# Optimization experiments

Measured on AMD Instinct MI355X. Metric: run time of the kernel, lower is better.

The kernel has to match this reference:

```python
import jax, jax.numpy as jnp
import numpy as np

D = 1024
H = 16
HD = D // H
FF = 4 * D
EPS = 1e-5


def _layernorm(x, g, s):
    m = x.mean(-1, keepdims=True)
    v = ((x - m) ** 2).mean(-1, keepdims=True)  # unbiased=False
    return g * (x - m) / jnp.sqrt(v + EPS) + s


def _gelu_tanh(x):
    c = jnp.sqrt(2.0 / jnp.pi).astype(x.dtype)
    return 0.5 * x * (1 + jnp.tanh(c * (x + 0.044715 * x ** 3)))


def setup_inputs() -> dict:
    key = jax.random.key(0)
    ks = jax.random.split(key, 12)
    B, T = 2, 2048
    std = 0.02
    x = jax.random.normal(ks[0], (B, T, D), jnp.float32)
    wq = jax.random.normal(ks[1], (D, D), jnp.float32) * std
    wk = jax.random.normal(ks[2], (D, D), jnp.float32) * std
    wv = jax.random.normal(ks[3], (D, D), jnp.float32) * std
    wo = jax.random.normal(ks[4], (D, D), jnp.float32) * std
    bo = jnp.zeros((D,), jnp.float32)
    w1 = jax.random.normal(ks[5], (FF, D), jnp.float32) * std
    b1 = jnp.zeros((FF,), jnp.float32)
    w2 = jax.random.normal(ks[6], (D, FF), jnp.float32) * std
    b2 = jnp.zeros((D,), jnp.float32)
    g1 = jnp.ones((D,), jnp.float32)
    s1 = jnp.zeros((D,), jnp.float32)
    g2 = jnp.ones((D,), jnp.float32)
    s2 = jnp.zeros((D,), jnp.float32)
    return {"x": x, "wq": wq, "wk": wk, "wv": wv, "wo": wo, "bo": bo,
            "w1": w1, "b1": b1, "w2": w2, "b2": b2,
            "g1": g1, "s1": s1, "g2": g2, "s2": s2}


def reference(x, wq, wk, wv, wo, bo, w1, b1, w2, b2, g1, s1, g2, s2):
    B, T, _ = x.shape
    # pre-LN attention
    h = _layernorm(x, g1, s1)
    q = (h @ wq.T).reshape(B, T, H, HD).transpose(0, 2, 1, 3)  # [B,H,T,HD]
    k = (h @ wk.T).reshape(B, T, H, HD).transpose(0, 2, 1, 3)
    v = (h @ wv.T).reshape(B, T, H, HD).transpose(0, 2, 1, 3)
    scores = jnp.einsum('bhqd,bhkd->bhqk', q, k)
    causal = jnp.triu(jnp.ones((T, T), bool), k=1)
    scores = jnp.where(causal, -jnp.inf, scores)
    attn = jax.nn.softmax(scores / jnp.sqrt(jnp.float32(HD)), axis=-1)
    ctx = jnp.einsum('bhqk,bhkd->bhqd', attn, v)
    ctx = ctx.transpose(0, 2, 1, 3).reshape(B, T, D)
    x = x + (ctx @ wo.T + bo)
    # pre-LN MLP
    h2 = _layernorm(x, g2, s2)
    ff = _gelu_tanh(h2 @ w1.T + b1) @ w2.T + b2
    return x + ff
```

## Files before the change

### kernel.cpp

```cpp
#include <hip/hip_runtime.h>
#include <hip/hip_bf16.h>
#include <stdint.h>


typedef __attribute__((ext_vector_type(8))) __bf16 bf16x8;
typedef __attribute__((ext_vector_type(4))) __bf16 bf16x4;
typedef __attribute__((ext_vector_type(4))) float  f32x4;

#define DD    1024
#define TSEQ  2048
#define NTOK  4096
#define FFD   4096

#define ASM_VMCNT0() asm volatile("s_waitcnt vmcnt(0)" ::: "memory")

__device__ __forceinline__ void gll16(const void* g, void* l) {
  __builtin_amdgcn_global_load_lds(
      (const __attribute__((address_space(1))) unsigned int*)g,
      (__attribute__((address_space(3))) unsigned int*)l, 16, 0, 0);
}

__device__ __forceinline__ float gelu_f(float v) {
  float u = 0.7978845608028654f * (v + 0.044715f * v * v * v);
  float t = 1.0f - 2.0f / (1.0f + __expf(2.0f * u));
  return 0.5f * v * (1.0f + t);
}

__global__ __launch_bounds__(256) void cvt_weights(
    const float* __restrict__ wq, const float* __restrict__ wk,
    const float* __restrict__ wv, const float* __restrict__ wo,
    const float* __restrict__ w1, const float* __restrict__ w2,
    __bf16* __restrict__ dst)
{
  size_t i4 = (size_t)blockIdx.x * 256 + threadIdx.x;
  size_t e = i4 * 4;
  const float* src; size_t off;
  if (e < (size_t)4 * 1048576) {
    int sel = (int)(e >> 20);
    src = sel == 0 ? wq : sel == 1 ? wk : sel == 2 ? wv : wo;
    off = e & 1048575;
  } else if (e < (size_t)8 * 1048576) {
    src = w1; off = e - (size_t)4 * 1048576;
  } else {
    src = w2; off = e - (size_t)8 * 1048576;
  }
  float4 v = *(const float4*)(src + off);
  bf16x4 o;
  o[0] = (__bf16)v.x; o[1] = (__bf16)v.y; o[2] = (__bf16)v.z; o[3] = (__bf16)v.w;
  *(bf16x4*)(dst + e) = o;
}

__global__ __launch_bounds__(256) void ln_kernel(
    const float* __restrict__ x, const float* __restrict__ gw,
    const float* __restrict__ sw, __bf16* __restrict__ out)
{
  const int row  = blockIdx.x * 4 + (threadIdx.x >> 6);
  const int lane = threadIdx.x & 63;
  const float4* xr = (const float4*)(x + (size_t)row * DD);
  float4 v[4];
  float s = 0.f, sq = 0.f;
#pragma unroll
  for (int i = 0; i < 4; ++i) {
    v[i] = xr[i * 64 + lane];
    s  += v[i].x + v[i].y + v[i].z + v[i].w;
    sq += v[i].x * v[i].x + v[i].y * v[i].y + v[i].z * v[i].z + v[i].w * v[i].w;
  }
#pragma unroll
  for (int off = 32; off >= 1; off >>= 1) {
    s  += __shfl_xor(s, off);
    sq += __shfl_xor(sq, off);
  }
  const float mean = s * (1.f / DD);
  const float rstd = rsqrtf(sq * (1.f / DD) - mean * mean + 1e-5f);
  const float4* gr = (const float4*)gw;
  const float4* sr = (const float4*)sw;
#pragma unroll
  for (int i = 0; i < 4; ++i) {
    float4 gv = gr[i * 64 + lane];
    float4 sv = sr[i * 64 + lane];
    bf16x4 o;
    o[0] = (__bf16)(gv.x * (v[i].x - mean) * rstd + sv.x);
    o[1] = (__bf16)(gv.y * (v[i].y - mean) * rstd + sv.y);
    o[2] = (__bf16)(gv.z * (v[i].z - mean) * rstd + sv.z);
    o[3] = (__bf16)(gv.w * (v[i].w - mean) * rstd + sv.w);
    *(bf16x4*)&out[(size_t)row * DD + (size_t)(i * 64 + lane) * 4] = o;
  }
}

template<int MODE>
__global__ __launch_bounds__(512, 2)
void gemm256(const __bf16* __restrict__ A, int lda,
             const __bf16* __restrict__ Bw, int ldb,
             __bf16* __restrict__ Cout, const float* __restrict__ bias,
             __bf16* __restrict__ voutT, int M, int N, int K)
{
  __shared__ __bf16 sm[65536];
  const int t = threadIdx.x;
  const int lane = t & 63;
  const int l15 = lane & 15, g = lane >> 4;
  const int w = t >> 6;
  const int wm = w >> 2, wn = w & 3;
  const int m0 = blockIdx.y * 256, n0 = blockIdx.x * 256;

  if (MODE == 2) {
    const int kz = blockIdx.z;
    A    += (size_t)kz * 1024;
    Bw   += (size_t)kz * 1024;
    Cout += (size_t)kz * (size_t)M * N;
  }

  const int srow = t >> 3;
  const int schunk = t & 7;
  const int gc = schunk ^ (srow & 7);
  const __bf16* gA = A  + (size_t)(m0 + srow) * lda + gc * 8;
  const __bf16* gB = Bw + (size_t)(n0 + srow) * ldb + gc * 8;
  char* smb = (char*)sm;
  const int sdst = t * 16;

  auto STAGE = [&](int kt, int cur) {
    char* dA = smb + cur * 65536;
    char* dB = dA + 32768;
    const __bf16* a = gA + kt * 64;
    const __bf16* b = gB + kt * 64;
#pragma unroll
    for (int i = 0; i < 4; ++i)
      gll16(a + (size_t)i * 64 * lda, dA + i * 8192 + sdst);
#pragma unroll
    for (int i = 0; i < 4; ++i)
      gll16(b + (size_t)i * 64 * ldb, dB + i * 8192 + sdst);
  };

  const int xa = l15 & 7;
  const int baseA0 = (wm * 128 + l15) * 128 + ((g ^ xa) << 4);
  const int baseA1 = (wm * 128 + l15) * 128 + (((4 + g) ^ xa) << 4);
  const int baseB0 = 32768 + (wn * 64 + l15) * 128 + ((g ^ xa) << 4);
  const int baseB1 = 32768 + (wn * 64 + l15) * 128 + (((4 + g) ^ xa) << 4);

  f32x4 acc[8][4] = {};
  const int NT = K >> 6;

  STAGE(0, 0);
  __syncthreads();

  for (int kt = 0; kt < NT; ++kt) {
    const int cur = kt & 1;
    if (kt + 1 < NT) STAGE(kt + 1, cur ^ 1);

    const char* bufb = smb + cur * 65536;
    bf16x8 af[8][2], bfr[4][2];
#pragma unroll
    for (int mi = 0; mi < 8; ++mi) {
      af[mi][0] = *(const bf16x8*)(bufb + baseA0 + mi * 2048);
      af[mi][1] = *(const bf16x8*)(bufb + baseA1 + mi * 2048);
    }
#pragma unroll
    for (int ni = 0; ni < 4; ++ni) {
      bfr[ni][0] = *(const bf16x8*)(bufb + baseB0 + ni * 2048);
      bfr[ni][1] = *(const bf16x8*)(bufb + baseB1 + ni * 2048);
    }
#pragma unroll
    for (int ks = 0; ks < 2; ++ks)
#pragma unroll
      for (int mi = 0; mi < 8; ++mi)
#pragma unroll
        for (int ni = 0; ni < 4; ++ni)
          acc[mi][ni] = __builtin_amdgcn_mfma_f32_16x16x32_bf16(
              af[mi][ks], bfr[ni][ks], acc[mi][ni], 0, 0, 0);

    __syncthreads();
  }

#pragma unroll
  for (int mi = 0; mi < 8; ++mi) {
    const int rr0 = m0 + wm * 128 + mi * 16 + 4 * g;
#pragma unroll
    for (int ni = 0; ni < 4; ++ni) {
      const int cc = n0 + wn * 64 + ni * 16 + l15;
      if (MODE == 0 && n0 + wn * 64 >= 2048) {
        const int b  = rr0 >> 11;
        const int t0 = rr0 & 2047;
        const int vc = cc - 2048;
        const int h = vc >> 6, d = vc & 63;
        bf16x4 o;
        o[0] = (__bf16)acc[mi][ni][0]; o[1] = (__bf16)acc[mi][ni][1];
        o[2] = (__bf16)acc[mi][ni][2]; o[3] = (__bf16)acc[mi][ni][3];
        *(bf16x4*)&voutT[(((size_t)(b * 16 + h)) * 64 + d) * 2048 + t0] = o;
      } else {
        const int ldc = (MODE == 0) ? 2048 : N;
#pragma unroll
        for (int r = 0; r < 4; ++r) {
          float v = acc[mi][ni][r];
          if (MODE == 0 && cc < 1024) v *= 0.125f;
          if (MODE == 1) { v += bias[cc]; v = gelu_f(v); }
          Cout[(size_t)(rr0 + r) * ldc + cc] = (__bf16)v;
        }
      }
    }
  }
}

__global__ __launch_bounds__(256) void ff2_reduce(
    const __bf16* __restrict__ part, const float* __restrict__ x2,
    const float* __restrict__ b2, float* __restrict__ out)
{
  const size_t e = ((size_t)blockIdx.x * 256 + threadIdx.x) * 4;
  float4 r = *(const float4*)(x2 + e);
  const float4 b = *(const float4*)(b2 + (e & 1023));
  r.x += b.x; r.y += b.y; r.z += b.z; r.w += b.w;
#pragma unroll
  for (int s = 0; s < 4; ++s) {
    bf16x4 p = *(const bf16x4*)(part + (size_t)s * 4194304 + e);
    r.x += (float)p[0]; r.y += (float)p[1]; r.z += (float)p[2]; r.w += (float)p[3];
  }
  *(float4*)(out + e) = r;
}

template<bool BIAS, bool RES>
__global__ __launch_bounds__(256, 3)
void gemm_bt(const __bf16* __restrict__ A, const __bf16* __restrict__ Bw,
             float* __restrict__ Cout, const float* __restrict__ bias,
             const float* __restrict__ res, int M, int N, int K)
{
  __shared__ __bf16 As[128 * 64];
  __shared__ __bf16 Bs[128 * 64];
  const int t    = threadIdx.x;
  const int lane = t & 63;
  const int l15  = lane & 15;
  const int g    = lane >> 4;
  const int w    = t >> 6;
  const int wr   = w >> 1, wc = w & 1;
  const int m0 = blockIdx.y * 128;
  const int n0 = blockIdx.x * 128;
  const int srow = t >> 3;
  const int scol = (t & 7) * 8;

  f32x4 acc[4][4] = {};
  const __bf16* Ap = A  + (size_t)m0 * K;
  const __bf16* Bp = Bw + (size_t)n0 * K;

  for (int k0 = 0; k0 < K; k0 += 64) {
#pragma unroll
    for (int i = 0; i < 4; ++i) {
      const int row = i * 32 + srow;
      gll16(Ap + (size_t)row * K + k0 + scol, &As[row * 64 + scol]);
    }
#pragma unroll
    for (int i = 0; i < 4; ++i) {
      const int row = i * 32 + srow;
      gll16(Bp + (size_t)row * K + k0 + scol, &Bs[row * 64 + scol]);
    }
    __syncthreads();
#pragma unroll
    for (int ks = 0; ks < 2; ++ks) {
      bf16x8 af[4], bfr[4];
#pragma unroll
      for (int mi = 0; mi < 4; ++mi)
        af[mi] = *(const bf16x8*)&As[(wr * 64 + mi * 16 + l15) * 64 + ks * 32 + g * 8];
#pragma unroll
      for (int ni = 0; ni < 4; ++ni)
        bfr[ni] = *(const bf16x8*)&Bs[(wc * 64 + ni * 16 + l15) * 64 + ks * 32 + g * 8];
#pragma unroll
      for (int mi = 0; mi < 4; ++mi)
#pragma unroll
        for (int ni = 0; ni < 4; ++ni)
          acc[mi][ni] = __builtin_amdgcn_mfma_f32_16x16x32_bf16(af[mi], bfr[ni], acc[mi][ni], 0, 0, 0);
    }
    __syncthreads();
  }

  const int crow0 = m0 + wr * 64;
  const int ccol0 = n0 + wc * 64;
#pragma unroll
  for (int mi = 0; mi < 4; ++mi) {
#pragma unroll
    for (int r = 0; r < 4; ++r) {
      const int rr = crow0 + mi * 16 + 4 * g + r;
#pragma unroll
      for (int ni = 0; ni < 4; ++ni) {
        const int cc = ccol0 + ni * 16 + l15;
        float v = acc[mi][ni][r];
        if (BIAS) v += bias[cc];
        if (RES)  v += res[(size_t)rr * N + cc];
        Cout[(size_t)rr * N + cc] = v;
      }
    }
  }
}

__device__ __forceinline__ void attn_tile(
    int kt, int qt, int qg,
    bf16x8 qf0, bf16x8 qf1,
    f32x4 (&acc)[4], float& mrun, float& lrun,
    char* pw, const char* KsB, const char* VTsB,
    int g, int l15, int xr)
{
  f32x4 s[4];
#pragma unroll
  for (int f = 0; f < 4; ++f) {
    const char* kb = KsB + (f * 16 + l15) * 128;
    bf16x8 a0 = *(const bf16x8*)(kb + ((g << 4) ^ xr));
    bf16x8 a1 = *(const bf16x8*)(kb + (((4 + g) << 4) ^ xr));
    f32x4 z = {};
    z = __builtin_amdgcn_mfma_f32_16x16x32_bf16(a0, qf0, z, 0, 0, 0);
    z = __builtin_amdgcn_mfma_f32_16x16x32_bf16(a1, qf1, z, 0, 0, 0);
    s[f] = z;
  }

  float pmax = -1e30f;
  if (kt == qt) {
#pragma unroll
    for (int f = 0; f < 4; ++f)
#pragma unroll
      for (int r = 0; r < 4; ++r) {
        const int kg = kt * 64 + f * 16 + g * 4 + r;
        if (kg > qg) s[f][r] = -1e30f;
        pmax = fmaxf(pmax, s[f][r]);
      }
  } else {
#pragma unroll
    for (int f = 0; f < 4; ++f)
#pragma unroll
      for (int r = 0; r < 4; ++r) pmax = fmaxf(pmax, s[f][r]);
  }
  pmax = fmaxf(pmax, __shfl_xor(pmax, 16));
  pmax = fmaxf(pmax, __shfl_xor(pmax, 32));

  if (__any(pmax > mrun)) {
    const float mnew  = fmaxf(mrun, pmax);
    const float alpha = __expf(mrun - mnew);
    float al[4];
#pragma unroll
    for (int r = 0; r < 4; ++r) al[r] = __shfl(alpha, g * 4 + r);
#pragma unroll
    for (int nf = 0; nf < 4; ++nf)
#pragma unroll
      for (int r = 0; r < 4; ++r) acc[nf][r] *= al[r];
    lrun *= alpha;
    mrun = mnew;
  }

  float lsum = 0.f;
#pragma unroll
  for (int f = 0; f < 4; ++f)
#pragma unroll
    for (int r = 0; r < 4; ++r) {
      float p = __expf(s[f][r] - mrun);
      s[f][r] = p;
      lsum += p;
    }
  lsum += __shfl_xor(lsum, 16);
  lsum += __shfl_xor(lsum, 32);
  lrun += lsum;

#pragma unroll
  for (int f = 0; f < 4; ++f) {
    bf16x4 pk;
    pk[0] = (__bf16)s[f][0]; pk[1] = (__bf16)s[f][1];
    pk[2] = (__bf16)s[f][2]; pk[3] = (__bf16)s[f][3];
    *(bf16x4*)(pw + ((((f * 2 + (g >> 1)) << 4) ^ xr) + (g & 1) * 8)) = pk;
  }
  asm volatile("s_waitcnt lgkmcnt(0)" ::: "memory");

#pragma unroll
  for (int ks = 0; ks < 2; ++ks) {
    bf16x8 pa = *(const bf16x8*)(pw + (((ks * 4 + g) << 4) ^ xr));
#pragma unroll
    for (int nf = 0; nf < 4; ++nf) {
      const char* vb = VTsB + (nf * 16 + l15) * 128;
      bf16x8 vf = *(const bf16x8*)(vb + (((ks * 4 + g) << 4) ^ xr));
      acc[nf] = __builtin_amdgcn_mfma_f32_16x16x32_bf16(pa, vf, acc[nf], 0, 0, 0);
    }
  }
}

__global__ __launch_bounds__(256, 2)
void attn_kernel(const __bf16* __restrict__ qk, const __bf16* __restrict__ vT,
                 __bf16* __restrict__ ctx)
{
  __shared__ __bf16 Ks[64 * 64];
  __shared__ __bf16 VTs[64 * 64];
  __shared__ __bf16 Ps[4][2][1024];
  const int t    = threadIdx.x;
  const int lane = t & 63;
  const int l15  = lane & 15;
  const int g    = lane >> 4;
  const int w    = t >> 6;
  const int j  = blockIdx.x;
  const int qtA = j, qtB = 31 - j;
  const int hh = blockIdx.y;
  const int bb = blockIdx.z;

  const int qrowA = qtA * 64 + w * 16 + l15;
  const int qrowB = qtB * 64 + w * 16 + l15;
  const size_t qkrA = ((size_t)(bb * 2048 + qrowA)) * 2048 + hh * 64;
  const size_t qkrB = ((size_t)(bb * 2048 + qrowB)) * 2048 + hh * 64;
  bf16x8 qfA0 = *(const bf16x8*)&qk[qkrA + g * 8];
  bf16x8 qfA1 = *(const bf16x8*)&qk[qkrA + 32 + g * 8];
  bf16x8 qfB0 = *(const bf16x8*)&qk[qkrB + g * 8];
  bf16x8 qfB1 = *(const bf16x8*)&qk[qkrB + 32 + g * 8];

  const int kk = t >> 2;
  const int c0 = (t & 3) * 16;
  const __bf16* kbase = &qk[((size_t)(bb * 2048) + kk) * 2048 + 1024 + hh * 64 + c0];
  const __bf16* vbase = &vT[(((size_t)(bb * 16 + hh)) * 64 + kk) * 2048 + c0];
  const int xw  = (kk & 7) << 4;
  char* kdst = (char*)Ks  + kk * 128;
  char* vdst = (char*)VTs + kk * 128;
  const int cw0 = ((((t & 3) * 2)    ) << 4) ^ xw;
  const int cw1 = ((((t & 3) * 2) + 1) << 4) ^ xw;

  f32x4 accA[4] = {}, accB[4] = {};
  float mA = -1e30f, lA = 0.f, mB = -1e30f, lB = 0.f;
  const int qgA = qtA * 64 + w * 16 + l15;
  const int qgB = qtB * 64 + w * 16 + l15;

  bf16x8 ka0, ka1, va0, va1, kb0, kb1, vb0, vb1;

  auto LOAD = [&](int kt, bf16x8& k0, bf16x8& k1, bf16x8& v0, bf16x8& v1) {
    const __bf16* kp = kbase + (size_t)kt * 64 * 2048;
    k0 = *(const bf16x8*)(kp);
    k1 = *(const bf16x8*)(kp + 8);
    const __bf16* vp = vbase + kt * 64;
    v0 = *(const bf16x8*)(vp);
    v1 = *(const bf16x8*)(vp + 8);
  };
  auto WRITE = [&](bf16x8& k0, bf16x8& k1, bf16x8& v0, bf16x8& v1) {
    *(bf16x8*)(kdst + cw0) = k0;
    *(bf16x8*)(kdst + cw1) = k1;
    *(bf16x8*)(vdst + cw0) = v0;
    *(bf16x8*)(vdst + cw1) = v1;
  };

  const int xr = (l15 & 7) << 4;
  char* pwA = (char*)&Ps[w][0][0] + l15 * 128;
  char* pwB = (char*)&Ps[w][1][0] + l15 * 128;
  const char* KsB  = (const char*)Ks;
  const char* VTsB = (const char*)VTs;

  const int NT = qtB + 1;
  LOAD(0, ka0, ka1, va0, va1);
  int kt = 0;
  for (;;) {
    ASM_VMCNT0();
    __syncthreads();
    WRITE(ka0, ka1, va0, va1);
    if (kt + 1 < NT) LOAD(kt + 1, kb0, kb1, vb0, vb1);
    __syncthreads();
    attn_tile(kt, qtB, qgB, qfB0, qfB1, accB, mB, lB, pwB, KsB, VTsB, g, l15, xr);
    if (kt <= qtA)
      attn_tile(kt, qtA, qgA, qfA0, qfA1, accA, mA, lA, pwA, KsB, VTsB, g, l15, xr);
    if (++kt >= NT) break;

    ASM_VMCNT0();
    __syncthreads();
    WRITE(kb0, kb1, vb0, vb1);
    if (kt + 1 < NT) LOAD(kt + 1, ka0, ka1, va0, va1);
    __syncthreads();
    attn_tile(kt, qtB, qgB, qfB0, qfB1, accB, mB, lB, pwB, KsB, VTsB, g, l15, xr);
    if (kt <= qtA)
      attn_tile(kt, qtA, qgA, qfA0, qfA1, accA, mA, lA, pwA, KsB, VTsB, g, l15, xr);
    if (++kt >= NT) break;
  }

  float liA[4], liB[4];
#pragma unroll
  for (int r = 0; r < 4; ++r) {
    liA[r] = 1.0f / __shfl(lA, g * 4 + r);
    liB[r] = 1.0f / __shfl(lB, g * 4 + r);
  }
#pragma unroll
  for (int nf = 0; nf < 4; ++nf)
#pragma unroll
    for (int r = 0; r < 4; ++r) {
      const int rowA = qtA * 64 + w * 16 + 4 * g + r;
      const int rowB = qtB * 64 + w * 16 + 4 * g + r;
      ctx[((size_t)(bb * 2048 + rowA)) * DD + hh * 64 + nf * 16 + l15] =
          (__bf16)(accA[nf][r] * liA[r]);
      ctx[((size_t)(bb * 2048 + rowB)) * DD + hh * 64 + nf * 16 + l15] =
          (__bf16)(accB[nf][r] * liB[r]);
    }
}

extern "C" void kernel_launch(void* const* d_in, const int* in_sizes, int n_in,
                              void* d_out, int out_size, void* d_ws, size_t ws_size,
                              hipStream_t stream)
{
  (void)in_sizes; (void)n_in; (void)out_size; (void)ws_size;
  const float* x  = (const float*)d_in[0];
  const float* wq = (const float*)d_in[1];
  const float* wk = (const float*)d_in[2];
  const float* wv = (const float*)d_in[3];
  const float* wo = (const float*)d_in[4];
  const float* bo = (const float*)d_in[5];
  const float* w1 = (const float*)d_in[6];
  const float* b1 = (const float*)d_in[7];
  const float* w2 = (const float*)d_in[8];
  const float* b2 = (const float*)d_in[9];
  const float* g1 = (const float*)d_in[10];
  const float* s1 = (const float*)d_in[11];
  const float* g2 = (const float*)d_in[12];
  const float* s2 = (const float*)d_in[13];
  float* out = (float*)d_out;

  char* ws = (char*)d_ws;
  __bf16* wbf  = (__bf16*)ws;
  __bf16* hbuf = (__bf16*)(ws + 25165824);
  __bf16* qkb  = (__bf16*)(ws + 33554432);
  __bf16* vbT  = (__bf16*)(ws + 50331648);
  __bf16* ctxb = (__bf16*)(ws + 58720256);
  float*  x2   = (float*)(ws + 67108864);
  __bf16* ffb  = (__bf16*)(ws + 83886080);
  __bf16* part = (__bf16*)(ws + 33554432);

  cvt_weights<<<12288, 256, 0, stream>>>(wq, wk, wv, wo, w1, w2, wbf);
  ln_kernel<<<1024, 256, 0, stream>>>(x, g1, s1, hbuf);

  gemm256<0><<<dim3(12, 16), 512, 0, stream>>>(
      hbuf, 1024, wbf, 1024, qkb, nullptr, vbT, NTOK, 3072, 1024);

  dim3 ga(16, 16, 2);
  attn_kernel<<<ga, 256, 0, stream>>>(qkb, vbT, ctxb);

  gemm_bt<true, true><<<dim3(8, 32), 256, 0, stream>>>(
      ctxb, wbf + 3145728, x2, bo, x, NTOK, DD, DD);
  ln_kernel<<<1024, 256, 0, stream>>>(x2, g2, s2, hbuf);

  gemm256<1><<<dim3(16, 16), 512, 0, stream>>>(
      hbuf, 1024, wbf + 4194304, 1024, ffb, b1, nullptr, NTOK, FFD, 1024);

  gemm256<2><<<dim3(4, 16, 4), 512, 0, stream>>>(
      ffb, 4096, wbf + 8388608, 4096, part, nullptr, nullptr, NTOK, DD, 1024);
  ff2_reduce<<<4096, 256, 0, stream>>>(part, x2, b2, out);
}
```

Baseline: 219.1 us.

## Replace 256-tile GEMMs for MLP and out-proj with swizzled 128-tile kernel

Adds a new 128x128-tile GEMM template with XOR-swizzled LDS layout and hoisted fragment loads. It replaces the unswizzled gemm_bt used for the output projection and the 256x256-tile gemm256 used for FF1 and FF2 split-K. The goal is fewer LDS bank conflicts and more blocks per wave for better CU occupancy. The cost is lower data reuse per tile and no double buffering in the new kernel.

```diff
diff --git a/kernel.cpp b/kernel.cpp
--- a/kernel.cpp
+++ b/kernel.cpp
@@ -101,13 +101,6 @@
   const int w = t >> 6;
   const int wm = w >> 2, wn = w & 3;
   const int m0 = blockIdx.y * 256, n0 = blockIdx.x * 256;
-
-  if (MODE == 2) {
-    const int kz = blockIdx.z;
-    A    += (size_t)kz * 1024;
-    Bw   += (size_t)kz * 1024;
-    Cout += (size_t)kz * (size_t)M * N;
-  }
 
   const int srow = t >> 3;
   const int schunk = t & 7;
@@ -186,14 +179,109 @@
         o[2] = (__bf16)acc[mi][ni][2]; o[3] = (__bf16)acc[mi][ni][3];
         *(bf16x4*)&voutT[(((size_t)(b * 16 + h)) * 64 + d) * 2048 + t0] = o;
       } else {
-        const int ldc = (MODE == 0) ? 2048 : N;
 #pragma unroll
         for (int r = 0; r < 4; ++r) {
           float v = acc[mi][ni][r];
           if (MODE == 0 && cc < 1024) v *= 0.125f;
-          if (MODE == 1) { v += bias[cc]; v = gelu_f(v); }
-          Cout[(size_t)(rr0 + r) * ldc + cc] = (__bf16)v;
+          Cout[(size_t)(rr0 + r) * 2048 + cc] = (__bf16)v;
         }
+      }
+    }
+  }
+}
+
+template<int MODE>
+__global__ __launch_bounds__(256, 4)
+void gemm128(const __bf16* __restrict__ A, int lda,
+             const __bf16* __restrict__ Bw, int ldb,
+             void* __restrict__ Cout, const float* __restrict__ bias,
+             const float* __restrict__ res, int M, int N, int K)
+{
+  __shared__ __bf16 sm[16384];
+  const int t = threadIdx.x;
+  const int lane = t & 63;
+  const int l15 = lane & 15, g = lane >> 4;
+  const int w = t >> 6;
+  const int wr = w >> 1, wc = w & 1;
+  const int m0 = blockIdx.y * 128, n0 = blockIdx.x * 128;
+
+  const __bf16* Ap = A;
+  const __bf16* Bp = Bw;
+  __bf16* Cb = (__bf16*)Cout;
+  if (MODE == 2) {
+    const int kz = blockIdx.z;
+    Ap += (size_t)kz * 1024;
+    Bp += (size_t)kz * 1024;
+    Cb += (size_t)kz * (size_t)M * N;
+  }
+
+  const int srow = t >> 3;
+  const int schunk = t & 7;
+  const int gc = schunk ^ (srow & 7);
+  const __bf16* gA = Ap + (size_t)(m0 + srow) * lda + gc * 8;
+  const __bf16* gB = Bp + (size_t)(n0 + srow) * ldb + gc * 8;
+  char* smb = (char*)sm;
+  const int sdst = t * 16;
+
+  const int xa = l15 & 7;
+  const int rA = (wr * 64 + l15) * 128;
+  const int rB = 16384 + (wc * 64 + l15) * 128;
+  const int baseA0 = rA + ((g ^ xa) << 4);
+  const int baseA1 = rA + (((4 + g) ^ xa) << 4);
+  const int baseB0 = rB + ((g ^ xa) << 4);
+  const int baseB1 = rB + (((4 + g) ^ xa) << 4);
+
+  f32x4 acc[4][4] = {};
+  const int NT = K >> 6;
+
+  for (int kt = 0; kt < NT; ++kt) {
+    const __bf16* a = gA + kt * 64;
+    const __bf16* b = gB + kt * 64;
+#pragma unroll
+    for (int i = 0; i < 4; ++i)
+      gll16(a + (size_t)i * 32 * lda, smb + i * 4096 + sdst);
+#pragma unroll
+    for (int i = 0; i < 4; ++i)
+      gll16(b + (size_t)i * 32 * ldb, smb + 16384 + i * 4096 + sdst);
+    __syncthreads();
+
+    bf16x8 af[4][2], bfr[4][2];
+#pragma unroll
+    for (int mi = 0; mi < 4; ++mi) {
+      af[mi][0] = *(const bf16x8*)(smb + baseA0 + mi * 2048);
+      af[mi][1] = *(const bf16x8*)(smb + baseA1 + mi * 2048);
+    }
+#pragma unroll
+    for (int ni = 0; ni < 4; ++ni) {
+      bfr[ni][0] = *(const bf16x8*)(smb + baseB0 + ni * 2048);
+      bfr[ni][1] = *(const bf16x8*)(smb + baseB1 + ni * 2048);
+    }
+#pragma unroll
+    for (int ks = 0; ks < 2; ++ks)
+#pragma unroll
+      for (int mi = 0; mi < 4; ++mi)
+#pragma unroll
+        for (int ni = 0; ni < 4; ++ni)
+          acc[mi][ni] = __builtin_amdgcn_mfma_f32_16x16x32_bf16(
+              af[mi][ks], bfr[ni][ks], acc[mi][ni], 0, 0, 0);
+
+    __syncthreads();
+  }
+
+#pragma unroll
+  for (int mi = 0; mi < 4; ++mi) {
+    const int rr0 = m0 + wr * 64 + mi * 16 + 4 * g;
+#pragma unroll
+    for (int ni = 0; ni < 4; ++ni) {
+      const int cc = n0 + wc * 64 + ni * 16 + l15;
+#pragma unroll
+      for (int r = 0; r < 4; ++r) {
+        float v = acc[mi][ni][r];
+        if (MODE == 1) { v += bias[cc]; v = gelu_f(v);
+                         Cb[(size_t)(rr0 + r) * N + cc] = (__bf16)v; }
+        if (MODE == 2) { Cb[(size_t)(rr0 + r) * N + cc] = (__bf16)v; }
+        if (MODE == 3) { v += bias[cc]; v += res[(size_t)(rr0 + r) * N + cc];
+                         ((float*)Cout)[(size_t)(rr0 + r) * N + cc] = v; }
       }
     }
   }
@@ -213,78 +301,6 @@
     r.x += (float)p[0]; r.y += (float)p[1]; r.z += (float)p[2]; r.w += (float)p[3];
   }
   *(float4*)(out + e) = r;
-}
-
-template<bool BIAS, bool RES>
-__global__ __launch_bounds__(256, 3)
-void gemm_bt(const __bf16* __restrict__ A, const __bf16* __restrict__ Bw,
-             float* __restrict__ Cout, const float* __restrict__ bias,
-             const float* __restrict__ res, int M, int N, int K)
-{
-  __shared__ __bf16 As[128 * 64];
-  __shared__ __bf16 Bs[128 * 64];
-  const int t    = threadIdx.x;
-  const int lane = t & 63;
-  const int l15  = lane & 15;
-  const int g    = lane >> 4;
-  const int w    = t >> 6;
-  const int wr   = w >> 1, wc = w & 1;
-  const int m0 = blockIdx.y * 128;
-  const int n0 = blockIdx.x * 128;
-  const int srow = t >> 3;
-  const int scol = (t & 7) * 8;
-
-  f32x4 acc[4][4] = {};
-  const __bf16* Ap = A  + (size_t)m0 * K;
-  const __bf16* Bp = Bw + (size_t)n0 * K;
-
-  for (int k0 = 0; k0 < K; k0 += 64) {
-#pragma unroll
-    for (int i = 0; i < 4; ++i) {
-      const int row = i * 32 + srow;
-      gll16(Ap + (size_t)row * K + k0 + scol, &As[row * 64 + scol]);
-    }
-#pragma unroll
-    for (int i = 0; i < 4; ++i) {
-      const int row = i * 32 + srow;
-      gll16(Bp + (size_t)row * K + k0 + scol, &Bs[row * 64 + scol]);
-    }
-    __syncthreads();
-#pragma unroll
-    for (int ks = 0; ks < 2; ++ks) {
-      bf16x8 af[4], bfr[4];
-#pragma unroll
-      for (int mi = 0; mi < 4; ++mi)
-        af[mi] = *(const bf16x8*)&As[(wr * 64 + mi * 16 + l15) * 64 + ks * 32 + g * 8];
-#pragma unroll
-      for (int ni = 0; ni < 4; ++ni)
-        bfr[ni] = *(const bf16x8*)&Bs[(wc * 64 + ni * 16 + l15) * 64 + ks * 32 + g * 8];
-#pragma unroll
-      for (int mi = 0; mi < 4; ++mi)
-#pragma unroll
-        for (int ni = 0; ni < 4; ++ni)
-          acc[mi][ni] = __builtin_amdgcn_mfma_f32_16x16x32_bf16(af[mi], bfr[ni], acc[mi][ni], 0, 0, 0);
-    }
-    __syncthreads();
-  }
-
-  const int crow0 = m0 + wr * 64;
-  const int ccol0 = n0 + wc * 64;
-#pragma unroll
-  for (int mi = 0; mi < 4; ++mi) {
-#pragma unroll
-    for (int r = 0; r < 4; ++r) {
-      const int rr = crow0 + mi * 16 + 4 * g + r;
-#pragma unroll
-      for (int ni = 0; ni < 4; ++ni) {
-        const int cc = ccol0 + ni * 16 + l15;
-        float v = acc[mi][ni][r];
-        if (BIAS) v += bias[cc];
-        if (RES)  v += res[(size_t)rr * N + cc];
-        Cout[(size_t)rr * N + cc] = v;
-      }
-    }
-  }
 }
 
 __device__ __forceinline__ void attn_tile(
@@ -521,14 +537,14 @@
   dim3 ga(16, 16, 2);
   attn_kernel<<<ga, 256, 0, stream>>>(qkb, vbT, ctxb);
 
-  gemm_bt<true, true><<<dim3(8, 32), 256, 0, stream>>>(
-      ctxb, wbf + 3145728, x2, bo, x, NTOK, DD, DD);
+  gemm128<3><<<dim3(8, 32), 256, 0, stream>>>(
+      ctxb, 1024, wbf + 3145728, 1024, x2, bo, x, NTOK, DD, 1024);
   ln_kernel<<<1024, 256, 0, stream>>>(x2, g2, s2, hbuf);
 
-  gemm256<1><<<dim3(16, 16), 512, 0, stream>>>(
+  gemm128<1><<<dim3(32, 32), 256, 0, stream>>>(
       hbuf, 1024, wbf + 4194304, 1024, ffb, b1, nullptr, NTOK, FFD, 1024);
 
-  gemm256<2><<<dim3(4, 16, 4), 512, 0, stream>>>(
+  gemm128<2><<<dim3(8, 32, 4), 256, 0, stream>>>(
       ffb, 4096, wbf + 8388608, 4096, part, nullptr, nullptr, NTOK, DD, 1024);
   ff2_reduce<<<4096, 256, 0, stream>>>(part, x2, b2, out);
 }
```

Result: slower. 229.2 us (+4.6%).
